# Kernel tuning notes

Measured on AMD Instinct MI355X. Metric: run time of the kernel, lower is better.

The kernel has to match this reference:

```python
import jax, jax.numpy as jnp
import numpy as np

U, T, Q, K, H = 2048, 200, 4096, 16, 256
STD_THETA = 1.0
LMDA_THETA = 1.0 / STD_THETA**2


def setup_inputs() -> dict:
    key = jax.random.key(0)
    ks = jax.random.split(key, 10)
    q_id = jax.random.randint(ks[0], (U, T), 0, Q)
    kmap = jax.random.bernoulli(ks[1], 0.25, (Q, K))
    mask = jnp.ones((U, T), dtype=bool)
    resp = jnp.round(jax.random.uniform(ks[2], (U, T))).astype(jnp.float32)
    diff_mu = jax.random.normal(ks[3], (Q,), jnp.float32) * 0.5
    disc_mu = jax.random.normal(ks[4], (Q,), jnp.float32) * 0.5
    W1 = jax.random.normal(ks[5], (3, H), jnp.float32) * 0.3
    b1 = jnp.zeros((H,), jnp.float32)
    W2 = jax.random.normal(ks[6], (H, H), jnp.float32) * (1.0 / np.sqrt(H))
    b2 = jnp.zeros((H,), jnp.float32)
    W3 = jax.random.normal(ks[7], (H, 2), jnp.float32) * (1.0 / np.sqrt(H))
    b3 = jnp.zeros((2,), jnp.float32)
    return dict(mask=mask, q_id=q_id, kmap=kmap, resp=resp,
                diff_mu=diff_mu, disc_mu=disc_mu,
                W1=W1, b1=b1, W2=W2, b2=b2, W3=W3, b3=b3)


def _gelu(x):
    return jax.nn.gelu(x, approximate=False)  # torch nn.GELU default (erf)


def reference(mask, q_id, kmap, resp, diff_mu, disc_mu, W1, b1, W2, b2, W3, b3):
    # --- per-trial potentials (MLP input is identical across the KC axis) ---
    td = diff_mu[q_id]                       # (U,T)  diff gather
    ts = disc_mu[q_id]                       # (U,T)  disc gather
    inp = jnp.stack([td, ts, resp], axis=-1)  # (U,T,3)
    h = _gelu(inp @ W1 + b1)
    h = _gelu(h @ W2 + b2)
    poten = _gelu(h @ W3 + b3)               # (U,T,2)
    mu = poten[..., 0]                       # (U,T)
    logvar = jnp.maximum(poten[..., 1], 1e-8)
    lmda = jnp.exp(-logvar)                  # (U,T)

    m = jnp.moveaxis(kmap[q_id], 1, 0)       # (T,U,K) trial KC mask
    mu_T = mu.T                              # (T,U)
    lmda_T = lmda.T                          # (T,U)
    zUK = jnp.zeros((mu.shape[0], m.shape[-1]), mu.dtype)  # (U,K)

    # --- backward (Kalman-style) alpha/beta recursion; unmasked slots carry ---
    def bwd(carry, xs):
        alpha, beta = carry                  # (U,K) each
        l, mu_, msk = xs                     # (U,), (U,), (U,K)
        l = l[:, None]
        mu_ = mu_[:, None]
        a_new = (l + alpha * LMDA_THETA) / (LMDA_THETA + l + alpha * LMDA_THETA)
        b_new = (l * mu_ + a_new * l * beta) / (l + a_new * l)
        alpha2 = jnp.where(msk, a_new, alpha)
        beta2 = jnp.where(msk, b_new, beta)
        return (alpha2, beta2), alpha2

    _, alphas = jax.lax.scan(bwd, (zUK, zUK), (lmda_T, mu_T, m), reverse=True)
    # alpha_next[t] = alpha_{t+1} (zero past the end)
    alpha_next = jnp.concatenate([alphas[1:], zUK[None]], axis=0)  # (T,U,K)

    # --- forward posterior-mean ability update (deterministic mean path) ---
    def fwd(ability, xs):
        l, mu_, msk, a_nxt = xs
        l = l[:, None]
        mu_ = mu_[:, None]
        b_nxt = a_nxt  # replicates original: beta_next = alpha_lst[t+1]
        mu_tilde = (LMDA_THETA * ability + mu_ * l + a_nxt * LMDA_THETA * b_nxt) \
                   / (LMDA_THETA + l + a_nxt * LMDA_THETA)
        ab = jnp.where(msk, mu_tilde, ability)  # masked scatter / carry-through
        return ab, ab

    _, ab_tk = jax.lax.scan(fwd, zUK, (lmda_T, mu_T, m, alpha_next))  # (T,U,K)

    mf = m.astype(mu.dtype)
    trial_ability = ((ab_tk * mf).sum(-1) / jnp.maximum(mf.sum(-1), 1e-8)).T  # (U,T)
    return trial_ability
```

## Files before the change

kernel.cpp:

```cpp
#include <hip/hip_runtime.h>
#include <hip/hip_bf16.h>
#include <stdint.h>

#define U_DIM 2048
#define T_DIM 200
#define Q_DIM 4096
#define K_DIM 16
#define H_DIM 256
#define N_ROWS (Q_DIM * 2)

typedef float f4 __attribute__((ext_vector_type(4)));
typedef float f2 __attribute__((ext_vector_type(2)));

__device__ __forceinline__ float gelu_f(float x) {
    return 0.5f * x * (1.0f + erff(x * 0.70710678118654752440f));
}

__global__ __launch_bounds__(256) void mlp_pack_kernel(
    const uint8_t* __restrict__ kmap, uint32_t* __restrict__ mask_tab,
    const float* __restrict__ diff_mu, const float* __restrict__ disc_mu,
    const float* __restrict__ W1, const float* __restrict__ b1,
    const float* __restrict__ W2, const float* __restrict__ b2,
    const float* __restrict__ W3, const float* __restrict__ b3,
    float* __restrict__ mu_tab, float* __restrict__ lmda_tab)
{
    __shared__ float h1t[H_DIM][20];
    __shared__ float red8[4][8][H_DIM];
    __shared__ uint32_t sflag;
    int tid  = threadIdx.x;
    int bid  = blockIdx.x;
    int row0 = bid * 16;

    if (bid < 16) {
        if (tid < 64) {
            const uint32_t* kw = (const uint32_t*)kmap;
            uint32_t any = 0;
            #pragma unroll
            for (int i = 0; i < 16; ++i) any |= (kw[tid + 64 * i] > 1u) ? 1u : 0u;
            uint64_t b = __ballot(any != 0);
            if (tid == 0) sflag = (b != 0) ? 1u : 0u;
        }
        __syncthreads();
        int q = bid * 256 + tid;
        uint32_t m = 0;
        if (sflag) {
            const uint32_t* p = (const uint32_t*)(kmap + (size_t)q * K_DIM);
            #pragma unroll
            for (int w = 0; w < 4; ++w) {
                uint32_t v = p[w];
                #pragma unroll
                for (int b = 0; b < 4; ++b)
                    m |= (((v >> (8 * b)) & 0xffu) ? 1u : 0u) << (4 * w + b);
            }
        } else {
            const int* ki = (const int*)kmap + (size_t)q * K_DIM;
            #pragma unroll
            for (int k = 0; k < K_DIM; ++k)
                m |= (ki[k] ? 1u : 0u) << k;
        }
        mask_tab[q] = m;
    }

    {
        int i = tid;
        float w1a = W1[i], w1b = W1[H_DIM + i], w1c = W1[2 * H_DIM + i], bi = b1[i];
        float hv[16];
        #pragma unroll
        for (int g = 0; g < 16; ++g) {
            int row = row0 + g;
            float td = diff_mu[row >> 1];
            float ts = disc_mu[row >> 1];
            float rr = (float)(row & 1);
            hv[g] = gelu_f(td * w1a + ts * w1b + rr * w1c + bi);
        }
        *(f4*)&h1t[i][0]  = (f4){hv[0],  hv[1],  hv[2],  hv[3]};
        *(f4*)&h1t[i][4]  = (f4){hv[4],  hv[5],  hv[6],  hv[7]};
        *(f4*)&h1t[i][8]  = (f4){hv[8],  hv[9],  hv[10], hv[11]};
        *(f4*)&h1t[i][12] = (f4){hv[12], hv[13], hv[14], hv[15]};
    }
    __syncthreads();

    int w = tid >> 6, l = tid & 63;
    float acc[16][4];
    #pragma unroll
    for (int g = 0; g < 16; ++g)
        acc[g][0] = acc[g][1] = acc[g][2] = acc[g][3] = 0.0f;
    #pragma unroll 4
    for (int s = 0; s < 64; ++s) {
        int i2 = 64 * w + s;
        f4 wv = *(const f4*)&W2[i2 * H_DIM + 4 * l];
        f4 hA = *(const f4*)&h1t[i2][0];
        f4 hB = *(const f4*)&h1t[i2][4];
        f4 hC = *(const f4*)&h1t[i2][8];
        f4 hD = *(const f4*)&h1t[i2][12];
        #pragma unroll
        for (int c = 0; c < 4; ++c) {
            acc[0][c]  += hA[0] * wv[c];
            acc[1][c]  += hA[1] * wv[c];
            acc[2][c]  += hA[2] * wv[c];
            acc[3][c]  += hA[3] * wv[c];
            acc[4][c]  += hB[0] * wv[c];
            acc[5][c]  += hB[1] * wv[c];
            acc[6][c]  += hB[2] * wv[c];
            acc[7][c]  += hB[3] * wv[c];
            acc[8][c]  += hC[0] * wv[c];
            acc[9][c]  += hC[1] * wv[c];
            acc[10][c] += hC[2] * wv[c];
            acc[11][c] += hC[3] * wv[c];
            acc[12][c] += hD[0] * wv[c];
            acc[13][c] += hD[1] * wv[c];
            acc[14][c] += hD[2] * wv[c];
            acc[15][c] += hD[3] * wv[c];
        }
    }

    f4 bb2  = *(const f4*)&b2[4 * l];
    f4 w3lo = *(const f4*)&W3[8 * l];
    f4 w3hi = *(const f4*)&W3[8 * l + 4];
    float bb30 = b3[0], bb31 = b3[1];
    #pragma unroll
    for (int phase = 0; phase < 2; ++phase) {
        int base = 8 * phase;
        __syncthreads();
        #pragma unroll
        for (int g = 0; g < 8; ++g)
            *(f4*)&red8[w][g][4 * l] =
                (f4){acc[base + g][0], acc[base + g][1], acc[base + g][2], acc[base + g][3]};
        __syncthreads();
        #pragma unroll
        for (int gg = 0; gg < 2; ++gg) {
            int g = 2 * w + gg;
            f4 s = bb2;
            #pragma unroll
            for (int ww = 0; ww < 4; ++ww) {
                f4 r = *(const f4*)&red8[ww][g][4 * l];
                s[0] += r[0]; s[1] += r[1]; s[2] += r[2]; s[3] += r[3];
            }
            float h0 = gelu_f(s[0]), h1v = gelu_f(s[1]),
                  h2v = gelu_f(s[2]), h3v = gelu_f(s[3]);
            float p0 = h0 * w3lo[0] + h1v * w3lo[2] + h2v * w3hi[0] + h3v * w3hi[2];
            float p1 = h0 * w3lo[1] + h1v * w3lo[3] + h2v * w3hi[1] + h3v * w3hi[3];
            #pragma unroll
            for (int off = 1; off < 64; off <<= 1) {
                p0 += __shfl_xor(p0, off);
                p1 += __shfl_xor(p1, off);
            }
            if (l == 0) {
                int row = row0 + base + g;
                mu_tab[row]   = gelu_f(p0 + bb30);
                lmda_tab[row] = expf(-fmaxf(gelu_f(p1 + bb31), 1e-8f));
            }
        }
    }
}

__global__ __launch_bounds__(64) void scan_fused_kernel(
    const int* __restrict__ q_id, const float* __restrict__ resp,
    const float* __restrict__ mu_tab, const float* __restrict__ lmda_tab,
    const uint32_t* __restrict__ mask_tab, float* __restrict__ out)
{
    __shared__ float a_lds[64][201];
    __shared__ f2 la_lds[4][T_DIM];
    __shared__ uint16_t mk_lds[4][T_DIM];
    int tid = threadIdx.x;
    int u0 = blockIdx.x * 4;

    int   qv[13];
    float rv[13];
    #pragma unroll
    for (int p = 0; p < 13; ++p) {
        int idx = tid + 64 * p;
        if (idx < 4 * T_DIM) {
            int ul = idx / T_DIM, t = idx - ul * T_DIM;
            int g = (u0 + ul) * T_DIM + t;
            qv[p] = q_id[g];
            rv[p] = resp[g];
        }
    }
    #pragma unroll
    for (int p = 0; p < 13; ++p) {
        int idx = tid + 64 * p;
        if (idx < 4 * T_DIM) {
            int ul = idx / T_DIM, t = idx - ul * T_DIM;
            int ix = 2 * qv[p] + (rv[p] != 0.0f ? 1 : 0);
            float l  = lmda_tab[ix];
            float mu = mu_tab[ix];
            la_lds[ul][t] = (f2){1.0f + l, mu * l};
            mk_lds[ul][t] = (uint16_t)mask_tab[qv[p]];
        }
    }
    __syncthreads();

    int ul = tid >> 4, k = tid & 15;
    float* ap = a_lds[tid];
    const f2* la = la_lds[ul];
    const uint16_t* mk = mk_lds[ul];

    float alpha = 0.0f;
    float L1s0 = la[196][0], L1s1 = la[197][0], L1s2 = la[198][0], L1s3 = la[199][0];
    uint32_t ms0 = mk[196], ms1 = mk[197], ms2 = mk[198], ms3 = mk[199];
    for (int tb = 196; tb >= 0; tb -= 4) {
        int p3 = (tb >= 1) ? tb - 1 : 0;
        int p2 = (tb >= 2) ? tb - 2 : 0;
        int p1 = (tb >= 3) ? tb - 3 : 0;
        int p0 = (tb >= 4) ? tb - 4 : 0;
        { float L1 = L1s3; uint32_t m = ms3; L1s3 = la[p3][0]; ms3 = mk[p3];
          ap[tb + 3] = alpha;
          float an = 1.0f - __builtin_amdgcn_rcpf(L1 + alpha);
          alpha = ((m >> k) & 1) ? an : alpha; }
        { float L1 = L1s2; uint32_t m = ms2; L1s2 = la[p2][0]; ms2 = mk[p2];
          ap[tb + 2] = alpha;
          float an = 1.0f - __builtin_amdgcn_rcpf(L1 + alpha);
          alpha = ((m >> k) & 1) ? an : alpha; }
        { float L1 = L1s1; uint32_t m = ms1; L1s1 = la[p1][0]; ms1 = mk[p1];
          ap[tb + 1] = alpha;
          float an = 1.0f - __builtin_amdgcn_rcpf(L1 + alpha);
          alpha = ((m >> k) & 1) ? an : alpha; }
        { float L1 = L1s0; uint32_t m = ms0; L1s0 = la[p0][0]; ms0 = mk[p0];
          ap[tb + 0] = alpha;
          float an = 1.0f - __builtin_amdgcn_rcpf(L1 + alpha);
          alpha = ((m >> k) & 1) ? an : alpha; }
    }

    float ability = 0.0f;
    f2 lv0 = la[0], lv1 = la[1], lv2 = la[2], lv3 = la[3];
    uint32_t n0 = mk[0], n1 = mk[1], n2 = mk[2], n3 = mk[3];
    float av0 = ap[0], av1 = ap[1], av2 = ap[2], av3 = ap[3];
    for (int tb = 0; tb < 200; tb += 4) {
        int p0 = (tb + 4 < 200) ? tb + 4 : 199;
        int p1 = (tb + 5 < 200) ? tb + 5 : 199;
        int p2 = (tb + 6 < 200) ? tb + 6 : 199;
        int p3 = (tb + 7 < 200) ? tb + 7 : 199;
        { f2 v = lv0; uint32_t m = n0; float a = av0;
          lv0 = la[p0]; n0 = mk[p0]; av0 = ap[p0];
          float r = __builtin_amdgcn_rcpf(v[0] + a);
          float c1 = v[1] + a * a;
          float mt = (ability + c1) * r;
          bool msk = (m >> k) & 1;
          ability = msk ? mt : ability;
          ap[tb + 0] = msk ? ability : 0.0f; }
        { f2 v = lv1; uint32_t m = n1; float a = av1;
          lv1 = la[p1]; n1 = mk[p1]; av1 = ap[p1];
          float r = __builtin_amdgcn_rcpf(v[0] + a);
          float c1 = v[1] + a * a;
          float mt = (ability + c1) * r;
          bool msk = (m >> k) & 1;
          ability = msk ? mt : ability;
          ap[tb + 1] = msk ? ability : 0.0f; }
        { f2 v = lv2; uint32_t m = n2; float a = av2;
          lv2 = la[p2]; n2 = mk[p2]; av2 = ap[p2];
          float r = __builtin_amdgcn_rcpf(v[0] + a);
          float c1 = v[1] + a * a;
          float mt = (ability + c1) * r;
          bool msk = (m >> k) & 1;
          ability = msk ? mt : ability;
          ap[tb + 2] = msk ? ability : 0.0f; }
        { f2 v = lv3; uint32_t m = n3; float a = av3;
          lv3 = la[p3]; n3 = mk[p3]; av3 = ap[p3];
          float r = __builtin_amdgcn_rcpf(v[0] + a);
          float c1 = v[1] + a * a;
          float mt = (ability + c1) * r;
          bool msk = (m >> k) & 1;
          ability = msk ? mt : ability;
          ap[tb + 3] = msk ? ability : 0.0f; }
    }
    __syncthreads();

    #pragma unroll
    for (int p = 0; p < 13; ++p) {
        int idx = tid + 64 * p;
        if (idx < 4 * T_DIM) {
            int uo = idx / T_DIM, t = idx - uo * T_DIM;
            float s = 0.0f;
            #pragma unroll
            for (int kk = 0; kk < 16; ++kk) s += a_lds[uo * 16 + kk][t];
            float c = (float)__popc((unsigned)(mk_lds[uo][t] & 0xffffu));
            out[(u0 + uo) * T_DIM + t] = s * __builtin_amdgcn_rcpf(fmaxf(c, 1e-8f));
        }
    }
}

extern "C" void kernel_launch(void* const* d_in, const int* in_sizes, int n_in,
                              void* d_out, int out_size, void* d_ws, size_t ws_size,
                              hipStream_t stream) {
    const int*     q_id    = (const int*)d_in[1];
    const uint8_t* kmap    = (const uint8_t*)d_in[2];
    const float*   resp    = (const float*)d_in[3];
    const float*   diff_mu = (const float*)d_in[4];
    const float*   disc_mu = (const float*)d_in[5];
    const float*   W1      = (const float*)d_in[6];
    const float*   b1      = (const float*)d_in[7];
    const float*   W2      = (const float*)d_in[8];
    const float*   b2      = (const float*)d_in[9];
    const float*   W3      = (const float*)d_in[10];
    const float*   b3      = (const float*)d_in[11];
    float* out = (float*)d_out;

    char* w = (char*)d_ws;
    float* mu_tab      = (float*)w;      w += (size_t)N_ROWS * 4;
    float* lmda_tab    = (float*)w;      w += (size_t)N_ROWS * 4;
    uint32_t* mask_tab = (uint32_t*)w;   w += (size_t)Q_DIM * 4;

    hipLaunchKernelGGL(mlp_pack_kernel, dim3(N_ROWS / 16), dim3(256), 0, stream,
                       kmap, mask_tab, diff_mu, disc_mu,
                       W1, b1, W2, b2, W3, b3, mu_tab, lmda_tab);
    hipLaunchKernelGGL(scan_fused_kernel, dim3(U_DIM / 4), dim3(64), 0, stream,
                       q_id, resp, mu_tab, lmda_tab, mask_tab, out);
}
```

Before: 119.7 us.

## Recast backward alpha recursion as projective fraction and vectorize LDS accesses

The backward alpha recursion alpha' = 1 - 1/(L1+alpha) is rewritten as a numerator/denominator (Möbius) update using only FMAs on the serial chain. Each step's alpha is obtained off the critical path via a reciprocal, with renormalisation every 8 steps. LDS reads and writes are widened to 128-bit vector loads of per-trial parameters, masks and alpha values, and the row stride is padded to 204 for alignment. This shortens the dependent latency chain in both scans, at the cost of extra reciprocals and possible bank conflicts from the new stride.

Result: faster. 115.4 us (-3.5%).

```diff
diff --git a/kernel.cpp b/kernel.cpp
--- a/kernel.cpp
+++ b/kernel.cpp
@@ -11,6 +11,7 @@
 
 typedef float f4 __attribute__((ext_vector_type(4)));
 typedef float f2 __attribute__((ext_vector_type(2)));
+typedef unsigned int u32x4 __attribute__((ext_vector_type(4)));
 
 __device__ __forceinline__ float gelu_f(float x) {
     return 0.5f * x * (1.0f + erff(x * 0.70710678118654752440f));
@@ -159,7 +160,7 @@
     const float* __restrict__ mu_tab, const float* __restrict__ lmda_tab,
     const uint32_t* __restrict__ mask_tab, float* __restrict__ out)
 {
-    __shared__ float a_lds[64][201];
+    __shared__ float a_lds[64][204];
     __shared__ f2 la_lds[4][T_DIM];
     __shared__ uint16_t mk_lds[4][T_DIM];
     int tid = threadIdx.x;
@@ -193,76 +194,77 @@
 
     int ul = tid >> 4, k = tid & 15;
     float* ap = a_lds[tid];
-    const f2* la = la_lds[ul];
-    const uint16_t* mk = mk_lds[ul];
-
-    float alpha = 0.0f;
-    float L1s0 = la[196][0], L1s1 = la[197][0], L1s2 = la[198][0], L1s3 = la[199][0];
-    uint32_t ms0 = mk[196], ms1 = mk[197], ms2 = mk[198], ms3 = mk[199];
-    for (int tb = 196; tb >= 0; tb -= 4) {
-        int p3 = (tb >= 1) ? tb - 1 : 0;
-        int p2 = (tb >= 2) ? tb - 2 : 0;
-        int p1 = (tb >= 3) ? tb - 3 : 0;
-        int p0 = (tb >= 4) ? tb - 4 : 0;
-        { float L1 = L1s3; uint32_t m = ms3; L1s3 = la[p3][0]; ms3 = mk[p3];
-          ap[tb + 3] = alpha;
-          float an = 1.0f - __builtin_amdgcn_rcpf(L1 + alpha);
-          alpha = ((m >> k) & 1) ? an : alpha; }
-        { float L1 = L1s2; uint32_t m = ms2; L1s2 = la[p2][0]; ms2 = mk[p2];
-          ap[tb + 2] = alpha;
-          float an = 1.0f - __builtin_amdgcn_rcpf(L1 + alpha);
-          alpha = ((m >> k) & 1) ? an : alpha; }
-        { float L1 = L1s1; uint32_t m = ms1; L1s1 = la[p1][0]; ms1 = mk[p1];
-          ap[tb + 1] = alpha;
-          float an = 1.0f - __builtin_amdgcn_rcpf(L1 + alpha);
-          alpha = ((m >> k) & 1) ? an : alpha; }
-        { float L1 = L1s0; uint32_t m = ms0; L1s0 = la[p0][0]; ms0 = mk[p0];
-          ap[tb + 0] = alpha;
-          float an = 1.0f - __builtin_amdgcn_rcpf(L1 + alpha);
-          alpha = ((m >> k) & 1) ? an : alpha; }
-    }
-
-    float ability = 0.0f;
-    f2 lv0 = la[0], lv1 = la[1], lv2 = la[2], lv3 = la[3];
-    uint32_t n0 = mk[0], n1 = mk[1], n2 = mk[2], n3 = mk[3];
-    float av0 = ap[0], av1 = ap[1], av2 = ap[2], av3 = ap[3];
-    for (int tb = 0; tb < 200; tb += 4) {
-        int p0 = (tb + 4 < 200) ? tb + 4 : 199;
-        int p1 = (tb + 5 < 200) ? tb + 5 : 199;
-        int p2 = (tb + 6 < 200) ? tb + 6 : 199;
-        int p3 = (tb + 7 < 200) ? tb + 7 : 199;
-        { f2 v = lv0; uint32_t m = n0; float a = av0;
-          lv0 = la[p0]; n0 = mk[p0]; av0 = ap[p0];
-          float r = __builtin_amdgcn_rcpf(v[0] + a);
-          float c1 = v[1] + a * a;
-          float mt = (ability + c1) * r;
-          bool msk = (m >> k) & 1;
-          ability = msk ? mt : ability;
-          ap[tb + 0] = msk ? ability : 0.0f; }
-        { f2 v = lv1; uint32_t m = n1; float a = av1;
-          lv1 = la[p1]; n1 = mk[p1]; av1 = ap[p1];
-          float r = __builtin_amdgcn_rcpf(v[0] + a);
-          float c1 = v[1] + a * a;
-          float mt = (ability + c1) * r;
-          bool msk = (m >> k) & 1;
-          ability = msk ? mt : ability;
-          ap[tb + 1] = msk ? ability : 0.0f; }
-        { f2 v = lv2; uint32_t m = n2; float a = av2;
-          lv2 = la[p2]; n2 = mk[p2]; av2 = ap[p2];
-          float r = __builtin_amdgcn_rcpf(v[0] + a);
-          float c1 = v[1] + a * a;
-          float mt = (ability + c1) * r;
-          bool msk = (m >> k) & 1;
-          ability = msk ? mt : ability;
-          ap[tb + 2] = msk ? ability : 0.0f; }
-        { f2 v = lv3; uint32_t m = n3; float a = av3;
-          lv3 = la[p3]; n3 = mk[p3]; av3 = ap[p3];
-          float r = __builtin_amdgcn_rcpf(v[0] + a);
-          float c1 = v[1] + a * a;
-          float mt = (ability + c1) * r;
-          bool msk = (m >> k) & 1;
-          ability = msk ? mt : ability;
-          ap[tb + 3] = msk ? ability : 0.0f; }
+    const f4*    laq = (const f4*)&la_lds[ul][0];
+    const u32x4* mkq = (const u32x4*)&mk_lds[ul][0];
+
+    {
+        float n = 0.0f, d = 1.0f;
+        f4 qa = laq[96], qb = laq[97], qc = laq[98], qd = laq[99];
+        u32x4 mw = mkq[24];
+        for (int gi = 24; gi >= 0; --gi) {
+            int tb = gi * 8;
+            int gp = (gi > 0) ? gi - 1 : 0;
+            f4 na = laq[gp * 4 + 0], nb = laq[gp * 4 + 1],
+               nc = laq[gp * 4 + 2], nd = laq[gp * 4 + 3];
+            u32x4 nw = mkq[gp];
+            float at0, at1, at2, at3, at4, at5, at6, at7;
+#define BSTEP(L1v, bitexpr, atv) { \
+            atv = n * __builtin_amdgcn_rcpf(d); \
+            float nn = fmaf((L1v) - 1.0f, d, n); \
+            float dd = fmaf((L1v), d, n); \
+            bool bb = (bitexpr); \
+            n = bb ? nn : n; d = bb ? dd : d; }
+            BSTEP(qd[2], (mw[3] >> (16 + k)) & 1, at7)
+            BSTEP(qd[0], (mw[3] >> k) & 1, at6)
+            BSTEP(qc[2], (mw[2] >> (16 + k)) & 1, at5)
+            BSTEP(qc[0], (mw[2] >> k) & 1, at4)
+            BSTEP(qb[2], (mw[1] >> (16 + k)) & 1, at3)
+            BSTEP(qb[0], (mw[1] >> k) & 1, at2)
+            BSTEP(qa[2], (mw[0] >> (16 + k)) & 1, at1)
+            BSTEP(qa[0], (mw[0] >> k) & 1, at0)
+#undef BSTEP
+            *(f4*)&ap[tb]     = (f4){at0, at1, at2, at3};
+            *(f4*)&ap[tb + 4] = (f4){at4, at5, at6, at7};
+            float s = __builtin_amdgcn_rcpf(d);
+            n *= s; d = 1.0f;
+            qa = na; qb = nb; qc = nc; qd = nd; mw = nw;
+        }
+    }
+
+    {
+        float ab = 0.0f;
+        f4 qa = laq[0], qb = laq[1], qc = laq[2], qd = laq[3];
+        u32x4 mw = mkq[0];
+        f4 av0 = *(const f4*)&ap[0], av1 = *(const f4*)&ap[4];
+        for (int gi = 0; gi < 25; ++gi) {
+            int tb = gi * 8;
+            int gp = (gi < 24) ? gi + 1 : 24;
+            f4 na = laq[gp * 4 + 0], nb = laq[gp * 4 + 1],
+               nc = laq[gp * 4 + 2], nd = laq[gp * 4 + 3];
+            u32x4 nw = mkq[gp];
+            f4 nv0 = *(const f4*)&ap[gp * 8], nv1 = *(const f4*)&ap[gp * 8 + 4];
+            float s0, s1, s2, s3, s4, s5, s6, s7;
+#define FSTEP(L1v, Av, aval, bitexpr, sv) { \
+            float r  = __builtin_amdgcn_rcpf((L1v) + (aval)); \
+            float cr = fmaf((aval), (aval), (Av)) * r; \
+            float mt = fmaf(ab, r, cr); \
+            bool bb = (bitexpr); \
+            ab = bb ? mt : ab; \
+            sv = bb ? ab : 0.0f; }
+            FSTEP(qa[0], qa[1], av0[0], (mw[0] >> k) & 1, s0)
+            FSTEP(qa[2], qa[3], av0[1], (mw[0] >> (16 + k)) & 1, s1)
+            FSTEP(qb[0], qb[1], av0[2], (mw[1] >> k) & 1, s2)
+            FSTEP(qb[2], qb[3], av0[3], (mw[1] >> (16 + k)) & 1, s3)
+            FSTEP(qc[0], qc[1], av1[0], (mw[2] >> k) & 1, s4)
+            FSTEP(qc[2], qc[3], av1[1], (mw[2] >> (16 + k)) & 1, s5)
+            FSTEP(qd[0], qd[1], av1[2], (mw[3] >> k) & 1, s6)
+            FSTEP(qd[2], qd[3], av1[3], (mw[3] >> (16 + k)) & 1, s7)
+#undef FSTEP
+            *(f4*)&ap[tb]     = (f4){s0, s1, s2, s3};
+            *(f4*)&ap[tb + 4] = (f4){s4, s5, s6, s7};
+            qa = na; qb = nb; qc = nc; qd = nd; mw = nw;
+            av0 = nv0; av1 = nv1;
+        }
     }
     __syncthreads();
 
```
